# Optimization experiments

Hardware: AMD Instinct MI355X
Metric: run time of the kernel (lower is better)

Reference implementation:

```python
import jax, jax.numpy as jnp
import numpy as np


def _inst(Xs, idx):
    # Xs: list of [N_type, D] feature tables, one per metapath position.
    # idx: [N, K, P] int indices. Returns max-pooled instance vectors [N, K, D].
    v = Xs[0][idx[..., 0]]
    for p in range(1, len(Xs)):
        v = jnp.maximum(v, Xs[p][idx[..., p]])
    return v


def _instance_attn(h, inst, W, a):
    # h: [N, D] target features; inst: [N, K, D]; W: [H, D, D]; a: [H, D].
    hi = jnp.einsum('nd,hde->hne', h, W)               # [H, N, D]
    hv = jnp.einsum('nkd,hde->hnke', inst, W)          # [H, N, K, D]
    e = jax.nn.leaky_relu(
        jnp.einsum('hnke,he->hnk', hv + hi[:, :, None, :], a), 0.2)
    alpha = jax.nn.softmax(e, axis=2)                  # softmax over K instances
    out = jnp.einsum('hnk,hnke->ne', alpha, hv)
    return out / W.shape[0]                            # mean over heads


def _metapath_attn(Hs, W, b, q):
    Hstk = jnp.stack(Hs)                               # [P, N, D]
    sem = jnp.tanh(Hstk @ W + b).mean(axis=1)          # [P, D]
    beta = jax.nn.softmax(jnp.sum(jnp.tanh(sem) * q, axis=1), axis=0)  # [P]
    return jnp.einsum('p,pnd->nd', beta, Hstk), beta


def setup_inputs() -> dict:
    N, D, K, H = 2048, 256, 20, 4
    key = jax.random.key(0)
    ks = iter(jax.random.split(key, 40))
    nrm = lambda shape, s=1.0: jax.random.normal(next(ks), shape, jnp.float32) * s
    ridx = lambda shape: jax.random.randint(next(ks), shape, 0, N, jnp.int32)
    w_s = 1.0 / np.sqrt(D).astype(np.float32)
    inp = {
        'X_drug': nrm((N, D)), 'X_dis': nrm((N, D)), 'X_gene': nrm((N, D)),
        'idx_rdr': ridx((N, K, 3)), 'idx_rdgdr': ridx((N, K, 5)),
        'idx_dgd': ridx((N, K, 3)), 'idx_drd': ridx((N, K, 3)),
        'idx_drrd': ridx((N, K, 4)), 'idx_gdrdg': ridx((N, K, 5)),
    }
    for mp in ['rdr', 'rdgdr', 'dgd', 'drd', 'drrd', 'gdrdg']:
        inp['W_' + mp] = nrm((H, D, D), w_s)
        inp['a_' + mp] = nrm((H, D), 0.01)
    for t in ['drug', 'dis', 'gene']:
        inp['Wm_' + t] = nrm((D, D), w_s)
        inp['bm_' + t] = jnp.zeros((D,), jnp.float32)
        inp['qm_' + t] = nrm((D,), 0.01)
    return inp


def reference(X_drug, X_dis, X_gene,
              idx_rdr, idx_rdgdr, idx_dgd, idx_drd, idx_drrd, idx_gdrdg,
              W_rdr, a_rdr, W_rdgdr, a_rdgdr, W_dgd, a_dgd, W_drd, a_drd,
              W_drrd, a_drrd, W_gdrdg, a_gdrdg,
              Wm_drug, bm_drug, qm_drug, Wm_dis, bm_dis, qm_dis,
              Wm_gene, bm_gene, qm_gene):
    # Drug metapaths: RDR, RDGDR
    H_rdr = _instance_attn(X_drug, _inst([X_drug, X_dis, X_drug], idx_rdr), W_rdr, a_rdr)
    H_rdgdr = _instance_attn(X_drug, _inst([X_drug, X_dis, X_gene, X_dis, X_drug], idx_rdgdr), W_rdgdr, a_rdgdr)
    H_drug, beta_drug = _metapath_attn([H_rdr, H_rdgdr], Wm_drug, bm_drug, qm_drug)
    # Disease metapaths: DGD, DRD, DRRD
    H_dgd = _instance_attn(X_dis, _inst([X_dis, X_gene, X_dis], idx_dgd), W_dgd, a_dgd)
    H_drd = _instance_attn(X_dis, _inst([X_dis, X_drug, X_dis], idx_drd), W_drd, a_drd)
    H_drrd = _instance_attn(X_dis, _inst([X_dis, X_drug, X_drug, X_dis], idx_drrd), W_drrd, a_drrd)
    H_dis, beta_dis = _metapath_attn([H_dgd, H_drd, H_drrd], Wm_dis, bm_dis, qm_dis)
    # Gene metapath: GDRDG
    H_gdrdg = _instance_attn(X_gene, _inst([X_gene, X_dis, X_drug, X_dis, X_gene], idx_gdrdg), W_gdrdg, a_gdrdg)
    H_gene, beta_gene = _metapath_attn([H_gdrdg], Wm_gene, bm_gene, qm_gene)
    return H_drug, H_dis, H_gene, beta_drug, beta_dis, beta_gene
```

## Files before the change

### kernel.cpp

```cpp
#include <hip/hip_runtime.h>
#include <math.h>

#define NN 2048
#define DD 256
#define KK 20
#define HH 4

typedef short short8 __attribute__((ext_vector_type(8)));
typedef float f32x4  __attribute__((ext_vector_type(4)));
typedef _Float16 half8 __attribute__((ext_vector_type(8)));
typedef _Float16 h2    __attribute__((ext_vector_type(2)));

#if defined(__has_builtin)
#  if __has_builtin(__builtin_amdgcn_fdot2)
#    define HAS_FDOT2 1
#  else
#    define HAS_FDOT2 0
#  endif
#else
#  define HAS_FDOT2 0
#endif

struct AllMP  { const unsigned short* xs[6][5]; const int* idx[6]; const unsigned short* xt[6]; int P[6]; };
struct SixPtr { const float* p[6]; };
struct SemB   { const unsigned short* Wmt[6]; const float* bm[6]; };

__device__ inline float wsum(float v){
  #pragma unroll
  for (int o=32;o;o>>=1) v += __shfl_xor(v,o);
  return v;
}
__device__ inline float gsum16(float v){
  #pragma unroll
  for (int o=8;o;o>>=1) v += __shfl_xor(v,o);
  return v;
}
__device__ inline unsigned short f2h(float x){
  return __builtin_bit_cast(unsigned short, (_Float16)x);
}
__device__ inline float h2f(unsigned short u){
  return (float)__builtin_bit_cast(_Float16, u);
}
__device__ inline h2 bch2(unsigned int u){ return __builtin_bit_cast(h2, u); }
__device__ inline unsigned int bcu(h2 v){ return __builtin_bit_cast(unsigned int, v); }
__device__ inline h2 packh2(float a, float b){ h2 r; r[0]=(_Float16)a; r[1]=(_Float16)b; return r; }
__device__ inline h2 hmax2(h2 a, h2 b){
  unsigned int d, ua = bcu(a), ub = bcu(b);
  asm("v_pk_max_f16 %0, %1, %2" : "=v"(d) : "v"(ua), "v"(ub));
  return bch2(d);
}
__device__ inline float dot2(h2 a, h2 b, float c){
#if HAS_FDOT2
  return __builtin_amdgcn_fdot2(a, b, c, false);
#else
  return c + (float)a[0]*(float)b[0] + (float)a[1]*(float)b[1];
#endif
}
__device__ inline void glds16(const void* g, void* l){
  __builtin_amdgcn_global_load_lds(
    (const __attribute__((address_space(1))) unsigned int*)g,
    (__attribute__((address_space(3))) unsigned int*)l, 16, 0, 0);
}

__launch_bounds__(256)
__global__ void prep_kernel(SixPtr W, SixPtr a, SixPtr Xp, SixPtr Wm3,
                            float* __restrict__ wa, unsigned short* __restrict__ Xh,
                            unsigned short* __restrict__ Wt, unsigned short* __restrict__ Wmt,
                            float* __restrict__ zero_base, int zero_cnt){
  __shared__ unsigned short T_s[64][68];
  int b = blockIdx.x;
  const int t = threadIdx.x;

  if (b < 24){
    if (b == 0){
      for (int i=t;i<zero_cnt;i+=256) zero_base[i] = 0.f;
    }
    const int m = b >> 2;
    const int local = ((b & 3) << 8) | t;
    const int h = local >> 8, d = local & 255;
    const float4* wrow = (const float4*)(W.p[m] + (size_t)(h*DD + d)*DD);
    const float4* av   = (const float4*)(a.p[m] + h*DD);
    float acc = 0.f;
    #pragma unroll 8
    for (int e=0;e<64;e++){
      float4 wv = wrow[e], xv = av[e];
      acc += wv.x*xv.x + wv.y*xv.y + wv.z*xv.z + wv.w*xv.w;
    }
    wa[m*1024 + local] = acc;
    return;
  }
  b -= 24;
  if (b < 1536){
    int gid = b*256 + t;
    int tb  = gid >> 17;
    int off = gid & 131071;
    float4 v = ((const float4*)Xp.p[tb])[off];
    ushort4 o = { f2h(v.x), f2h(v.y), f2h(v.z), f2h(v.w) };
    ((ushort4*)(Xh + (size_t)tb*NN*DD))[off] = o;
    return;
  }
  b -= 1536;
  const float* src; unsigned short* ob; int R, C, r0, c0;
  if (b < 384){
    int m = b/64, rem = b%64;
    src = W.p[m]; ob = Wt + (size_t)m*256*1024;
    R = 1024; C = 256; r0 = (rem>>2)*64; c0 = (rem&3)*64;
  } else {
    int bb = b-384;
    int m = bb/16, rem = bb%16;
    src = Wm3.p[m]; ob = Wmt + (size_t)m*256*256;
    R = 256; C = 256; r0 = (rem>>2)*64; c0 = (rem&3)*64;
  }
  {
    const int rr = t>>4, cc = (t&15)*4;
    #pragma unroll
    for (int i=0;i<4;i++){
      float4 v = *(const float4*)(src + (size_t)(r0+rr+i*16)*C + c0 + cc);
      T_s[cc+0][rr+i*16]=f2h(v.x);
      T_s[cc+1][rr+i*16]=f2h(v.y);
      T_s[cc+2][rr+i*16]=f2h(v.z);
      T_s[cc+3][rr+i*16]=f2h(v.w);
    }
    __syncthreads();
    const int cr = t>>4, rc = (t&15)*4;
    #pragma unroll
    for (int i=0;i<4;i++){
      int c = c0 + cr + i*16;
      ushort4 v = { T_s[cr+i*16][rc+0], T_s[cr+i*16][rc+1],
                    T_s[cr+i*16][rc+2], T_s[cr+i*16][rc+3] };
      int col = (r0 + rc) ^ ((c&7)<<3);
      *(ushort4*)(ob + (size_t)c*R + col) = v;
    }
  }
}

template<int P>
__device__ inline void inst_core(const AllMP& mp, int m, int n, int l,
                                 const float* __restrict__ wa_all,
                                 unsigned int (*inst_lds)[128], float (*alpha_lds)[4],
                                 unsigned short* __restrict__ ctxh){
  const int g = l >> 4;
  const int j = l & 15;
  const int* __restrict__ gidx = mp.idx[m] + (size_t)n*(KK*P);

  h2 wh[8];
  {
    const float4* wab = (const float4*)(wa_all + m*1024 + g*256);
    #pragma unroll
    for (int c=0;c<4;c++){
      float4 wv = wab[j + 16*c];
      wh[2*c]   = packh2(wv.x, wv.y);
      wh[2*c+1] = packh2(wv.z, wv.w);
    }
  }

  float sg;
  {
    const uint2* xb = (const uint2*)(mp.xt[m] + (size_t)n*DD);
    float p_ = 0.f;
    #pragma unroll
    for (int c=0;c<4;c++){
      uint2 rr = xb[j + 16*c];
      p_ = dot2(bch2(rr.x), wh[2*c+0], p_);
      p_ = dot2(bch2(rr.y), wh[2*c+1], p_);
    }
    sg = gsum16(p_);
  }

  unsigned int v0[KK], v1[KK];
  #pragma unroll
  for (int k=0;k<KK;k++){
    h2 a, bb;
    {
      int id = gidx[k*P];
      const uint2* rp = (const uint2*)(mp.xs[m][0] + (size_t)id*DD);
      uint2 r = rp[l];
      a = bch2(r.x); bb = bch2(r.y);
    }
    #pragma unroll
    for (int p=1;p<P;p++){
      int id = gidx[k*P+p];
      const uint2* rp = (const uint2*)(mp.xs[m][p] + (size_t)id*DD);
      uint2 u = rp[l];
      a = hmax2(a, bch2(u.x)); bb = hmax2(bb, bch2(u.y));
    }
    v0[k] = bcu(a); v1[k] = bcu(bb);
    *(uint2*)&inst_lds[k][2*l] = make_uint2(v0[k], v1[k]);
  }

  float e[KK];
  #pragma unroll
  for (int k=0;k<KK;k++){
    float pr = 0.f;
    #pragma unroll
    for (int c=0;c<4;c++){
      uint2 rr = *(const uint2*)&inst_lds[k][2*(j+16*c)];
      pr = dot2(bch2(rr.x), wh[2*c+0], pr);
      pr = dot2(bch2(rr.y), wh[2*c+1], pr);
    }
    pr = gsum16(pr);
    float logit = pr + sg;
    e[k] = (logit>0.f) ? logit : 0.2f*logit;
  }

  float mx = e[0];
  #pragma unroll
  for (int k=1;k<KK;k++) mx = fmaxf(mx, e[k]);
  float s = 0.f;
  #pragma unroll
  for (int k=0;k<KK;k++){ e[k] = __expf(e[k]-mx); s += e[k]; }
  float inv = 1.0f/s;
  #pragma unroll
  for (int k=0;k<KK;k++) e[k] *= inv;
  if (j==0){
    #pragma unroll
    for (int k=0;k<KK;k++) alpha_lds[k][g] = e[k];
  }

  float c[4][4] = {};
  #pragma unroll
  for (int k=0;k<KK;k++){
    float4 af = *(const float4*)&alpha_lds[k][0];
    h2 x0 = bch2(v0[k]), x1 = bch2(v1[k]);
    float f0=(float)x0[0], f1=(float)x0[1], f2=(float)x1[0], f3=(float)x1[1];
    c[0][0]+=af.x*f0; c[0][1]+=af.x*f1; c[0][2]+=af.x*f2; c[0][3]+=af.x*f3;
    c[1][0]+=af.y*f0; c[1][1]+=af.y*f1; c[1][2]+=af.y*f2; c[1][3]+=af.y*f3;
    c[2][0]+=af.z*f0; c[2][1]+=af.z*f1; c[2][2]+=af.z*f2; c[2][3]+=af.z*f3;
    c[3][0]+=af.w*f0; c[3][1]+=af.w*f1; c[3][2]+=af.w*f2; c[3][3]+=af.w*f3;
  }

  unsigned short* cb = ctxh + ((size_t)m*NN + n)*1024;
  const int col = (4*l) ^ ((n&7)<<3);
  #pragma unroll
  for (int h=0;h<4;h++){
    ushort4 o = { f2h(c[h][0]), f2h(c[h][1]), f2h(c[h][2]), f2h(c[h][3]) };
    *(ushort4*)(cb + h*DD + col) = o;
  }
}

__launch_bounds__(64)
__global__ void inst_attn_kernel(AllMP mp, const float* __restrict__ wa_all,
                                 unsigned short* __restrict__ ctxh){
  __shared__ unsigned int inst_lds[KK][128];
  __shared__ float alpha_lds[KK][4];
  const int m = blockIdx.y;
  const int n = blockIdx.x;
  const int l = threadIdx.x;
  switch(mp.P[m]){
    case 3: inst_core<3>(mp,m,n,l,wa_all,inst_lds,alpha_lds,ctxh); break;
    case 4: inst_core<4>(mp,m,n,l,wa_all,inst_lds,alpha_lds,ctxh); break;
    default: inst_core<5>(mp,m,n,l,wa_all,inst_lds,alpha_lds,ctxh); break;
  }
}

__launch_bounds__(256)
__global__ void gemm_kernel(const unsigned short* __restrict__ ctxh,
                            const unsigned short* __restrict__ Wt,
                            unsigned short* __restrict__ Hmp){
  __shared__ unsigned short A_s[2][64][64];
  __shared__ unsigned short B_s[2][64][64];
  const int m  = blockIdx.z;
  const int n0 = blockIdx.x*64, c0 = blockIdx.y*64;
  const int t  = threadIdx.x;
  const int l  = t & 63;
  const int wid  = t >> 6;
  const int wrow = wid & 1, wcol = wid >> 1;
  const unsigned short* Abase = ctxh + (size_t)m*NN*1024;
  const unsigned short* Bbase = Wt   + (size_t)m*256*1024;

  f32x4 acc[2][2] = {};
  const int row8 = l>>3, seg = l&7;

  {
    #pragma unroll
    for (int i=0;i<2;i++){
      const int r = wid*16 + i*8;
      glds16(Abase + (size_t)(n0+r+row8)*1024 + 0 + seg*8, &A_s[0][r][0]);
      glds16(Bbase + (size_t)(c0+r+row8)*1024 + 0 + seg*8, &B_s[0][r][0]);
    }
  }
  __syncthreads();

  #pragma unroll 2
  for (int it=0; it<16; it++){
    const int buf = it&1;
    if (it<15){
      const int k0 = (it+1)*64;
      #pragma unroll
      for (int i=0;i<2;i++){
        const int r = wid*16 + i*8;
        glds16(Abase + (size_t)(n0+r+row8)*1024 + k0 + seg*8, &A_s[buf^1][r][0]);
        glds16(Bbase + (size_t)(c0+r+row8)*1024 + k0 + seg*8, &B_s[buf^1][r][0]);
      }
    }
    __builtin_amdgcn_s_setprio(1);
    #pragma unroll
    for (int kf=0;kf<2;kf++){
      half8 a[2], b[2];
      const int s = kf*4 + (l>>4);
      #pragma unroll
      for (int mr=0;mr<2;mr++){
        const int row = wrow*32 + mr*16 + (l&15);
        a[mr] = __builtin_bit_cast(half8, *(const short8*)&A_s[buf][row][(s ^ (row&7))*8]);
      }
      #pragma unroll
      for (int nr=0;nr<2;nr++){
        const int col = wcol*32 + nr*16 + (l&15);
        b[nr] = __builtin_bit_cast(half8, *(const short8*)&B_s[buf][col][(s ^ (col&7))*8]);
      }
      #pragma unroll
      for (int mr=0;mr<2;mr++)
        #pragma unroll
        for (int nr=0;nr<2;nr++)
          acc[mr][nr] = __builtin_amdgcn_mfma_f32_16x16x32_f16(a[mr], b[nr], acc[mr][nr], 0,0,0);
    }
    __builtin_amdgcn_s_setprio(0);
    __syncthreads();
  }

  unsigned short* out = Hmp + (size_t)m*NN*DD;
  #pragma unroll
  for (int mr=0;mr<2;mr++){
    const int rbase = n0 + wrow*32 + mr*16 + (l>>4)*4;
    #pragma unroll
    for (int nr=0;nr<2;nr++){
      const int col = c0 + wcol*32 + nr*16 + (l&15);
      #pragma unroll
      for (int r=0;r<4;r++){
        const int rw = rbase + r;
        out[(size_t)rw*DD + (col ^ ((rw&7)<<3))] = f2h(acc[mr][nr][r]*0.25f);
      }
    }
  }
}

__launch_bounds__(256)
__global__ void sem_kernel(const unsigned short* __restrict__ Hmp, SemB sb,
                           float* __restrict__ sem_sum){
  __shared__ unsigned short A_s[64][256];
  __shared__ unsigned short B_s[64][256];
  const int m  = blockIdx.z;
  const int n0 = blockIdx.x*64, c0 = blockIdx.y*64;
  const int t  = threadIdx.x, l = t & 63, wid = t >> 6;
  const int wrow = wid & 1, wcol = wid >> 1;
  const unsigned short* Ab = Hmp + (size_t)m*NN*DD;
  const unsigned short* Bb = sb.Wmt[m];

  const int row2 = l>>5, seg = l&31;
  #pragma unroll
  for (int i=0;i<8;i++){
    const int r = wid*16 + i*2;
    glds16(Ab + (size_t)(n0+r+row2)*DD + seg*8, &A_s[r][0]);
    glds16(Bb + (size_t)(c0+r+row2)*DD + seg*8, &B_s[r][0]);
  }
  __syncthreads();

  f32x4 acc[2][2] = {};
  #pragma unroll
  for (int kf=0; kf<8; kf++){
    const int s = kf*4 + (l>>4);
    half8 a[2], b[2];
    #pragma unroll
    for (int mr=0;mr<2;mr++){
      int row = wrow*32 + mr*16 + (l&15);
      int ss = (s&24) | ((s&7)^(row&7));
      a[mr] = __builtin_bit_cast(half8, *(const short8*)((const char*)&A_s[0][0] + row*512 + ss*16));
    }
    #pragma unroll
    for (int nr=0;nr<2;nr++){
      int row = wcol*32 + nr*16 + (l&15);
      int ss = (s&24) | ((s&7)^(row&7));
      b[nr] = __builtin_bit_cast(half8, *(const short8*)((const char*)&B_s[0][0] + row*512 + ss*16));
    }
    #pragma unroll
    for (int mr=0;mr<2;mr++)
      #pragma unroll
      for (int nr=0;nr<2;nr++)
        acc[mr][nr] = __builtin_amdgcn_mfma_f32_16x16x32_f16(a[mr], b[nr], acc[mr][nr], 0,0,0);
  }

  #pragma unroll
  for (int nr=0;nr<2;nr++){
    const int col = c0 + wcol*32 + nr*16 + (l&15);
    float b = sb.bm[m][col];
    float sv = 0.f;
    #pragma unroll
    for (int mr=0;mr<2;mr++)
      #pragma unroll
      for (int r=0;r<4;r++)
        sv += tanhf(acc[mr][nr][r] + b);
    sv += __shfl_xor(sv,16);
    sv += __shfl_xor(sv,32);
    if (l < 16) atomicAdd(&sem_sum[m*DD + col], sv);
  }
}

__launch_bounds__(256)
__global__ void combine_kernel(const unsigned short* __restrict__ Hmp,
                               const float* __restrict__ sem_sum,
                               const float* __restrict__ qm0, const float* __restrict__ qm1,
                               const float* __restrict__ qm2,
                               float* __restrict__ out){
  const int type = blockIdx.y;
  const int start = (type==0) ? 0 : (type==1) ? 2 : 5;
  const int P = (type==0) ? 2 : (type==1) ? 3 : 1;
  const float* qm = (type==0) ? qm0 : (type==1) ? qm1 : qm2;
  const int t = threadIdx.x;
  __shared__ float red[3][4];
  __shared__ float beta_s[3];

  float q = qm[t];
  #pragma unroll
  for (int p=0;p<3;p++){
    if (p < P){
      float sm = sem_sum[(start+p)*DD + t] * (1.0f/NN);
      float v = wsum(tanhf(sm)*q);
      if ((t&63)==0) red[p][t>>6] = v;
    }
  }
  __syncthreads();
  if (t==0){
    float logits[3], e[3];
    float mx = -INFINITY;
    #pragma unroll
    for (int p=0;p<3;p++){
      if (p < P){
        logits[p] = red[p][0]+red[p][1]+red[p][2]+red[p][3];
        mx = fmaxf(mx, logits[p]);
      }
    }
    float s = 0.f;
    #pragma unroll
    for (int p=0;p<3;p++){
      if (p < P){ e[p] = __expf(logits[p]-mx); s += e[p]; }
    }
    #pragma unroll
    for (int p=0;p<3;p++)
      if (p < P) beta_s[p] = e[p]/s;
  }
  __syncthreads();

  if (blockIdx.x==0 && t<P)
    out[(size_t)3*NN*DD + start + t] = beta_s[t];

  const int n0 = blockIdx.x*4;
  #pragma unroll
  for (int r=0;r<4;r++){
    const int n = n0 + r;
    const int ds = t ^ ((n&7)<<3);
    const unsigned short* base = Hmp + ((size_t)start*NN + n)*DD + ds;
    float acc = 0.f;
    #pragma unroll
    for (int p=0;p<3;p++)
      if (p < P) acc += beta_s[p]*h2f(base[(size_t)p*NN*DD]);
    out[((size_t)type*NN + n)*DD + t] = acc;
  }
}

extern "C" void kernel_launch(void* const* d_in, const int* in_sizes, int n_in,
                              void* d_out, int out_size, void* d_ws, size_t ws_size,
                              hipStream_t stream) {
  SixPtr Xp; Xp.p[0]=(const float*)d_in[0]; Xp.p[1]=(const float*)d_in[1]; Xp.p[2]=(const float*)d_in[2];
  for (int i=3;i<6;i++) Xp.p[i]=Xp.p[0];

  SixPtr Wl, al;
  for (int m=0;m<6;m++){ Wl.p[m] = (const float*)d_in[9+2*m]; al.p[m] = (const float*)d_in[10+2*m]; }
  const float* Wm_[3]; const float* bm_[3]; const float* qm_[3];
  for (int tt=0;tt<3;tt++){
    Wm_[tt] = (const float*)d_in[21+3*tt];
    bm_[tt] = (const float*)d_in[22+3*tt];
    qm_[tt] = (const float*)d_in[23+3*tt];
  }
  SixPtr Wm3; for (int i=0;i<6;i++) Wm3.p[i] = Wm_[i<3?i:0];

  char* ws = (char*)d_ws;
  float* wa_all  = (float*)ws;                               ws += 6*1024*4;
  float* sem_sum = (float*)ws;                               ws += 6*DD*4;
  unsigned short* Hmp  = (unsigned short*)ws;                ws += (size_t)6*NN*DD*2;
  unsigned short* Wt   = (unsigned short*)ws;                ws += (size_t)6*256*1024*2;
  unsigned short* Wmt  = (unsigned short*)ws;                ws += (size_t)3*256*256*2;
  unsigned short* Xh   = (unsigned short*)ws;                ws += (size_t)3*NN*DD*2;
  unsigned short* ctxh = (unsigned short*)ws;

  AllMP mp;
  for (int m=0;m<6;m++) mp.idx[m] = (const int*)d_in[3+m];
  const int P_[6] = {3,5,3,3,4,5};
  for (int m=0;m<6;m++) mp.P[m] = P_[m];
  const int xt_t[6] = {0,0,1,1,1,2};
  const int gp_t[6][5] = {
    {0,1,0,0,0}, {0,1,2,1,0}, {1,2,1,1,1},
    {1,0,1,1,1}, {1,0,0,1,1}, {2,1,0,1,2}};
  for (int m=0;m<6;m++){
    mp.xt[m] = Xh + (size_t)xt_t[m]*NN*DD;
    for (int p=0;p<5;p++) mp.xs[m][p] = Xh + (size_t)gp_t[m][p]*NN*DD;
  }

  SemB sb;
  const int type_of[6] = {0,0,1,1,1,2};
  for (int m=0;m<6;m++){
    sb.Wmt[m] = Wmt + (size_t)type_of[m]*256*256;
    sb.bm[m]  = bm_[type_of[m]];
  }

  prep_kernel<<<dim3(24+1536+384+48),dim3(256),0,stream>>>(
      Wl, al, Xp, Wm3, wa_all, Xh, Wt, Wmt, sem_sum, 6*DD);

  inst_attn_kernel<<<dim3(NN,6),dim3(64),0,stream>>>(mp, wa_all, ctxh);
  gemm_kernel<<<dim3(32,4,6),dim3(256),0,stream>>>(ctxh, Wt, Hmp);
  sem_kernel<<<dim3(32,4,6),dim3(256),0,stream>>>(Hmp, sb, sem_sum);

  float* out = (float*)d_out;
  combine_kernel<<<dim3(NN/4,3),dim3(256),0,stream>>>(Hmp, sem_sum, qm_[0], qm_[1], qm_[2], out);
}
```

Before: 91.21 us.

## Stream instance attention over K chunks with unnormalized softmax accumulation

The kernel now processes the 20 instances in chunks of 5 through a double-buffered LDS chunk and accumulates exp-weighted context on the fly, normalizing by per-head sums only at the end. It no longer subtracts a running max before exponentiating. This drops the per-thread v0/v1/e arrays to cut register pressure and LDS size, which should allow higher occupancy and more gather overlap. The missing max subtraction risks overflow if the logits are large, and chunking limits how many gathers are in flight at once.

```diff
diff --git a/kernel.cpp b/kernel.cpp
--- a/kernel.cpp
+++ b/kernel.cpp
@@ -4,6 +4,7 @@
 #define NN 2048
 #define DD 256
 #define KK 20
+#define KCH 5
 #define HH 4
 
 typedef short short8 __attribute__((ext_vector_type(8)));
@@ -137,7 +138,8 @@
 template<int P>
 __device__ inline void inst_core(const AllMP& mp, int m, int n, int l,
                                  const float* __restrict__ wa_all,
-                                 unsigned int (*inst_lds)[128], float (*alpha_lds)[4],
+                                 uint2 (*chunk)[KCH][64],
+                                 float (*e_s)[KCH][4],
                                  unsigned short* __restrict__ ctxh){
   const int g = l >> 4;
   const int j = l & 15;
@@ -167,89 +169,89 @@
     sg = gsum16(p_);
   }
 
-  unsigned int v0[KK], v1[KK];
-  #pragma unroll
-  for (int k=0;k<KK;k++){
-    h2 a, bb;
-    {
-      int id = gidx[k*P];
-      const uint2* rp = (const uint2*)(mp.xs[m][0] + (size_t)id*DD);
-      uint2 r = rp[l];
-      a = bch2(r.x); bb = bch2(r.y);
-    }
-    #pragma unroll
-    for (int p=1;p<P;p++){
-      int id = gidx[k*P+p];
-      const uint2* rp = (const uint2*)(mp.xs[m][p] + (size_t)id*DD);
-      uint2 u = rp[l];
-      a = hmax2(a, bch2(u.x)); bb = hmax2(bb, bch2(u.y));
-    }
-    v0[k] = bcu(a); v1[k] = bcu(bb);
-    *(uint2*)&inst_lds[k][2*l] = make_uint2(v0[k], v1[k]);
-  }
-
-  float e[KK];
-  #pragma unroll
-  for (int k=0;k<KK;k++){
-    float pr = 0.f;
-    #pragma unroll
-    for (int c=0;c<4;c++){
-      uint2 rr = *(const uint2*)&inst_lds[k][2*(j+16*c)];
-      pr = dot2(bch2(rr.x), wh[2*c+0], pr);
-      pr = dot2(bch2(rr.y), wh[2*c+1], pr);
-    }
-    pr = gsum16(pr);
-    float logit = pr + sg;
-    e[k] = (logit>0.f) ? logit : 0.2f*logit;
-  }
-
-  float mx = e[0];
-  #pragma unroll
-  for (int k=1;k<KK;k++) mx = fmaxf(mx, e[k]);
-  float s = 0.f;
-  #pragma unroll
-  for (int k=0;k<KK;k++){ e[k] = __expf(e[k]-mx); s += e[k]; }
-  float inv = 1.0f/s;
-  #pragma unroll
-  for (int k=0;k<KK;k++) e[k] *= inv;
-  if (j==0){
-    #pragma unroll
-    for (int k=0;k<KK;k++) alpha_lds[k][g] = e[k];
-  }
-
+  float s0=0.f, s1=0.f, s2=0.f, s3=0.f;
   float c[4][4] = {};
-  #pragma unroll
-  for (int k=0;k<KK;k++){
-    float4 af = *(const float4*)&alpha_lds[k][0];
-    h2 x0 = bch2(v0[k]), x1 = bch2(v1[k]);
-    float f0=(float)x0[0], f1=(float)x0[1], f2=(float)x1[0], f3=(float)x1[1];
-    c[0][0]+=af.x*f0; c[0][1]+=af.x*f1; c[0][2]+=af.x*f2; c[0][3]+=af.x*f3;
-    c[1][0]+=af.y*f0; c[1][1]+=af.y*f1; c[1][2]+=af.y*f2; c[1][3]+=af.y*f3;
-    c[2][0]+=af.z*f0; c[2][1]+=af.z*f1; c[2][2]+=af.z*f2; c[2][3]+=af.z*f3;
-    c[3][0]+=af.w*f0; c[3][1]+=af.w*f1; c[3][2]+=af.w*f2; c[3][3]+=af.w*f3;
-  }
+
+  #pragma unroll
+  for (int ch=0; ch<KK/KCH; ch++){
+    const int par = ch & 1;
+    #pragma unroll
+    for (int kk=0; kk<KCH; kk++){
+      const int k = ch*KCH + kk;
+      h2 a, bb;
+      {
+        int id = gidx[k*P];
+        const uint2* rp = (const uint2*)(mp.xs[m][0] + (size_t)id*DD);
+        uint2 r = rp[l];
+        a = bch2(r.x); bb = bch2(r.y);
+      }
+      #pragma unroll
+      for (int p=1;p<P;p++){
+        int id = gidx[k*P+p];
+        const uint2* rp = (const uint2*)(mp.xs[m][p] + (size_t)id*DD);
+        uint2 u = rp[l];
+        a = hmax2(a, bch2(u.x)); bb = hmax2(bb, bch2(u.y));
+      }
+      chunk[par][kk][l] = make_uint2(bcu(a), bcu(bb));
+    }
+    #pragma unroll
+    for (int kk=0; kk<KCH; kk++){
+      float pr = 0.f;
+      #pragma unroll
+      for (int cidx=0;cidx<4;cidx++){
+        uint2 rr = chunk[par][kk][j + 16*cidx];
+        pr = dot2(bch2(rr.x), wh[2*cidx+0], pr);
+        pr = dot2(bch2(rr.y), wh[2*cidx+1], pr);
+      }
+      pr = gsum16(pr);
+      if (j==0){
+        float logit = pr + sg;
+        e_s[par][kk][g] = (logit>0.f) ? logit : 0.2f*logit;
+      }
+    }
+    #pragma unroll
+    for (int kk=0; kk<KCH; kk++){
+      float4 e4 = *(const float4*)&e_s[par][kk][0];
+      float w0=__expf(e4.x), w1=__expf(e4.y), w2=__expf(e4.z), w3=__expf(e4.w);
+      s0+=w0; s1+=w1; s2+=w2; s3+=w3;
+      uint2 xv = chunk[par][kk][l];
+      h2 x0 = bch2(xv.x), x1 = bch2(xv.y);
+      float f0=(float)x0[0], f1=(float)x0[1], f2=(float)x1[0], f3=(float)x1[1];
+      c[0][0]+=w0*f0; c[0][1]+=w0*f1; c[0][2]+=w0*f2; c[0][3]+=w0*f3;
+      c[1][0]+=w1*f0; c[1][1]+=w1*f1; c[1][2]+=w1*f2; c[1][3]+=w1*f3;
+      c[2][0]+=w2*f0; c[2][1]+=w2*f1; c[2][2]+=w2*f2; c[2][3]+=w2*f3;
+      c[3][0]+=w3*f0; c[3][1]+=w3*f1; c[3][2]+=w3*f2; c[3][3]+=w3*f3;
+    }
+  }
+
+  const float i0=1.f/s0, i1=1.f/s1, i2=1.f/s2, i3=1.f/s3;
 
   unsigned short* cb = ctxh + ((size_t)m*NN + n)*1024;
   const int col = (4*l) ^ ((n&7)<<3);
-  #pragma unroll
-  for (int h=0;h<4;h++){
-    ushort4 o = { f2h(c[h][0]), f2h(c[h][1]), f2h(c[h][2]), f2h(c[h][3]) };
-    *(ushort4*)(cb + h*DD + col) = o;
+  {
+    ushort4 o0 = { f2h(c[0][0]*i0), f2h(c[0][1]*i0), f2h(c[0][2]*i0), f2h(c[0][3]*i0) };
+    ushort4 o1 = { f2h(c[1][0]*i1), f2h(c[1][1]*i1), f2h(c[1][2]*i1), f2h(c[1][3]*i1) };
+    ushort4 o2 = { f2h(c[2][0]*i2), f2h(c[2][1]*i2), f2h(c[2][2]*i2), f2h(c[2][3]*i2) };
+    ushort4 o3 = { f2h(c[3][0]*i3), f2h(c[3][1]*i3), f2h(c[3][2]*i3), f2h(c[3][3]*i3) };
+    *(ushort4*)(cb + 0*DD + col) = o0;
+    *(ushort4*)(cb + 1*DD + col) = o1;
+    *(ushort4*)(cb + 2*DD + col) = o2;
+    *(ushort4*)(cb + 3*DD + col) = o3;
   }
 }
 
 __launch_bounds__(64)
 __global__ void inst_attn_kernel(AllMP mp, const float* __restrict__ wa_all,
                                  unsigned short* __restrict__ ctxh){
-  __shared__ unsigned int inst_lds[KK][128];
-  __shared__ float alpha_lds[KK][4];
+  __shared__ uint2 chunk[2][KCH][64];
+  __shared__ float e_s[2][KCH][4];
   const int m = blockIdx.y;
   const int n = blockIdx.x;
   const int l = threadIdx.x;
   switch(mp.P[m]){
-    case 3: inst_core<3>(mp,m,n,l,wa_all,inst_lds,alpha_lds,ctxh); break;
-    case 4: inst_core<4>(mp,m,n,l,wa_all,inst_lds,alpha_lds,ctxh); break;
-    default: inst_core<5>(mp,m,n,l,wa_all,inst_lds,alpha_lds,ctxh); break;
+    case 3: inst_core<3>(mp,m,n,l,wa_all,chunk,e_s,ctxh); break;
+    case 4: inst_core<4>(mp,m,n,l,wa_all,chunk,e_s,ctxh); break;
+    default: inst_core<5>(mp,m,n,l,wa_all,chunk,e_s,ctxh); break;
   }
 }
 
```

After: 118.2 us. +29.6%, slower.

## Compute instance attention logits with MFMA instead of fdot2 reductions

Applied to the files above, without the earlier changes.

Replaces the per-instance fdot2 dot products and 16-lane shuffle reductions for attention logits with two 16x16x32 f16 MFMAs. The 20 pooled instance vectors plus the target row are staged in padded LDS and multiplied against a zero-padded f16 copy of W·a, which prep_kernel now writes. Softmax is then computed over the MFMA accumulator layout with cross-lane shuffles. This trades scalar dot work for matrix-core work, at the cost of extra LDS staging, a wider padded weight buffer and more complex lane indexing.

```diff
diff --git a/kernel.cpp b/kernel.cpp
--- a/kernel.cpp
+++ b/kernel.cpp
@@ -11,16 +11,6 @@
 typedef _Float16 half8 __attribute__((ext_vector_type(8)));
 typedef _Float16 h2    __attribute__((ext_vector_type(2)));
 
-#if defined(__has_builtin)
-#  if __has_builtin(__builtin_amdgcn_fdot2)
-#    define HAS_FDOT2 1
-#  else
-#    define HAS_FDOT2 0
-#  endif
-#else
-#  define HAS_FDOT2 0
-#endif
-
 struct AllMP  { const unsigned short* xs[6][5]; const int* idx[6]; const unsigned short* xt[6]; int P[6]; };
 struct SixPtr { const float* p[6]; };
 struct SemB   { const unsigned short* Wmt[6]; const float* bm[6]; };
@@ -30,11 +20,6 @@
   for (int o=32;o;o>>=1) v += __shfl_xor(v,o);
   return v;
 }
-__device__ inline float gsum16(float v){
-  #pragma unroll
-  for (int o=8;o;o>>=1) v += __shfl_xor(v,o);
-  return v;
-}
 __device__ inline unsigned short f2h(float x){
   return __builtin_bit_cast(unsigned short, (_Float16)x);
 }
@@ -42,19 +27,10 @@
   return (float)__builtin_bit_cast(_Float16, u);
 }
 __device__ inline h2 bch2(unsigned int u){ return __builtin_bit_cast(h2, u); }
-__device__ inline unsigned int bcu(h2 v){ return __builtin_bit_cast(unsigned int, v); }
-__device__ inline h2 packh2(float a, float b){ h2 r; r[0]=(_Float16)a; r[1]=(_Float16)b; return r; }
-__device__ inline h2 hmax2(h2 a, h2 b){
-  unsigned int d, ua = bcu(a), ub = bcu(b);
+__device__ inline unsigned int umax2(unsigned int ua, unsigned int ub){
+  unsigned int d;
   asm("v_pk_max_f16 %0, %1, %2" : "=v"(d) : "v"(ua), "v"(ub));
-  return bch2(d);
-}
-__device__ inline float dot2(h2 a, h2 b, float c){
-#if HAS_FDOT2
-  return __builtin_amdgcn_fdot2(a, b, c, false);
-#else
-  return c + (float)a[0]*(float)b[0] + (float)a[1]*(float)b[1];
-#endif
+  return d;
 }
 __device__ inline void glds16(const void* g, void* l){
   __builtin_amdgcn_global_load_lds(
@@ -64,7 +40,8 @@
 
 __launch_bounds__(256)
 __global__ void prep_kernel(SixPtr W, SixPtr a, SixPtr Xp, SixPtr Wm3,
-                            float* __restrict__ wa, unsigned short* __restrict__ Xh,
+                            float* __restrict__ wa, unsigned short* __restrict__ wah,
+                            unsigned short* __restrict__ Xh,
                             unsigned short* __restrict__ Wt, unsigned short* __restrict__ Wmt,
                             float* __restrict__ zero_base, int zero_cnt){
   __shared__ unsigned short T_s[64][68];
@@ -87,6 +64,10 @@
       acc += wv.x*xv.x + wv.y*xv.y + wv.z*xv.z + wv.w*xv.w;
     }
     wa[m*1024 + local] = acc;
+    wah[(size_t)m*4096 + local] = f2h(acc);
+    wah[(size_t)m*4096 + 1024 + local] = 0;
+    wah[(size_t)m*4096 + 2048 + local] = 0;
+    wah[(size_t)m*4096 + 3072 + local] = 0;
     return;
   }
   b -= 24;
@@ -136,85 +117,78 @@
 
 template<int P>
 __device__ inline void inst_core(const AllMP& mp, int m, int n, int l,
-                                 const float* __restrict__ wa_all,
-                                 unsigned int (*inst_lds)[128], float (*alpha_lds)[4],
+                                 const unsigned short* __restrict__ wah,
+                                 unsigned short* inst_lds,
+                                 float (*alpha_lds)[4],
                                  unsigned short* __restrict__ ctxh){
-  const int g = l >> 4;
-  const int j = l & 15;
   const int* __restrict__ gidx = mp.idx[m] + (size_t)n*(KK*P);
 
-  h2 wh[8];
-  {
-    const float4* wab = (const float4*)(wa_all + m*1024 + g*256);
-    #pragma unroll
-    for (int c=0;c<4;c++){
-      float4 wv = wab[j + 16*c];
-      wh[2*c]   = packh2(wv.x, wv.y);
-      wh[2*c+1] = packh2(wv.z, wv.w);
-    }
-  }
-
-  float sg;
-  {
-    const uint2* xb = (const uint2*)(mp.xt[m] + (size_t)n*DD);
-    float p_ = 0.f;
-    #pragma unroll
-    for (int c=0;c<4;c++){
-      uint2 rr = xb[j + 16*c];
-      p_ = dot2(bch2(rr.x), wh[2*c+0], p_);
-      p_ = dot2(bch2(rr.y), wh[2*c+1], p_);
-    }
-    sg = gsum16(p_);
-  }
-
   unsigned int v0[KK], v1[KK];
   #pragma unroll
   for (int k=0;k<KK;k++){
-    h2 a, bb;
+    unsigned int a, bb;
     {
       int id = gidx[k*P];
-      const uint2* rp = (const uint2*)(mp.xs[m][0] + (size_t)id*DD);
-      uint2 r = rp[l];
-      a = bch2(r.x); bb = bch2(r.y);
+      uint2 r = ((const uint2*)(mp.xs[m][0] + (size_t)id*DD))[l];
+      a = r.x; bb = r.y;
     }
     #pragma unroll
     for (int p=1;p<P;p++){
       int id = gidx[k*P+p];
-      const uint2* rp = (const uint2*)(mp.xs[m][p] + (size_t)id*DD);
-      uint2 u = rp[l];
-      a = hmax2(a, bch2(u.x)); bb = hmax2(bb, bch2(u.y));
-    }
-    v0[k] = bcu(a); v1[k] = bcu(bb);
-    *(uint2*)&inst_lds[k][2*l] = make_uint2(v0[k], v1[k]);
-  }
-
-  float e[KK];
-  #pragma unroll
-  for (int k=0;k<KK;k++){
-    float pr = 0.f;
-    #pragma unroll
-    for (int c=0;c<4;c++){
-      uint2 rr = *(const uint2*)&inst_lds[k][2*(j+16*c)];
-      pr = dot2(bch2(rr.x), wh[2*c+0], pr);
-      pr = dot2(bch2(rr.y), wh[2*c+1], pr);
-    }
-    pr = gsum16(pr);
-    float logit = pr + sg;
-    e[k] = (logit>0.f) ? logit : 0.2f*logit;
-  }
-
-  float mx = e[0];
-  #pragma unroll
-  for (int k=1;k<KK;k++) mx = fmaxf(mx, e[k]);
-  float s = 0.f;
-  #pragma unroll
-  for (int k=0;k<KK;k++){ e[k] = __expf(e[k]-mx); s += e[k]; }
-  float inv = 1.0f/s;
-  #pragma unroll
-  for (int k=0;k<KK;k++) e[k] *= inv;
-  if (j==0){
-    #pragma unroll
-    for (int k=0;k<KK;k++) alpha_lds[k][g] = e[k];
+      uint2 u = ((const uint2*)(mp.xs[m][p] + (size_t)id*DD))[l];
+      a = umax2(a, u.x); bb = umax2(bb, u.y);
+    }
+    v0[k] = a; v1[k] = bb;
+    *(uint2*)(inst_lds + k*264 + 4*l) = make_uint2(a, bb);
+  }
+  {
+    uint2 xt = ((const uint2*)(mp.xt[m] + (size_t)n*DD))[l];
+    *(uint2*)(inst_lds + 20*264 + 4*l) = xt;
+  }
+
+  f32x4 acc0 = {}, acc1 = {};
+  {
+    const int r = l & 15, qc = (l>>4)*8;
+    const unsigned short* wb = wah + (size_t)m*4096 + (size_t)(l&15)*256;
+    #pragma unroll
+    for (int s=0;s<8;s++){
+      half8 a0 = __builtin_bit_cast(half8, *(const short8*)(inst_lds + r*264      + s*32 + qc));
+      half8 a1 = __builtin_bit_cast(half8, *(const short8*)(inst_lds + (16+r)*264 + s*32 + qc));
+      half8 bf = __builtin_bit_cast(half8, *(const short8*)(wb + s*32 + qc));
+      acc0 = __builtin_amdgcn_mfma_f32_16x16x32_f16(a0, bf, acc0, 0,0,0);
+      acc1 = __builtin_amdgcn_mfma_f32_16x16x32_f16(a1, bf, acc1, 0,0,0);
+    }
+  }
+
+  const int col = l & 15, q = l >> 4;
+  float sgv = __shfl(acc1[0], 16 + col);
+  float lg[4], lg2[4];
+  #pragma unroll
+  for (int r=0;r<4;r++){
+    float x = acc0[r] + sgv; lg[r]  = (x>0.f) ? x : 0.2f*x;
+    float y = acc1[r] + sgv; lg2[r] = (y>0.f) ? y : 0.2f*y;
+  }
+  float mx  = fmaxf(fmaxf(lg[0],lg[1]), fmaxf(lg[2],lg[3]));
+  float mx2 = fmaxf(fmaxf(lg2[0],lg2[1]), fmaxf(lg2[2],lg2[3]));
+  mx = fmaxf(mx, (q==0) ? mx2 : -INFINITY);
+  mx = fmaxf(mx, __shfl_xor(mx,16));
+  mx = fmaxf(mx, __shfl_xor(mx,32));
+  float ex[4], ex2[4], s = 0.f;
+  #pragma unroll
+  for (int r=0;r<4;r++){ ex[r] = __expf(lg[r]-mx); s += ex[r]; }
+  #pragma unroll
+  for (int r=0;r<4;r++)  ex2[r] = __expf(lg2[r]-mx);
+  if (q==0) s += ex2[0]+ex2[1]+ex2[2]+ex2[3];
+  s += __shfl_xor(s,16);
+  s += __shfl_xor(s,32);
+  const float inv = 1.f/s;
+  if (col < HH){
+    #pragma unroll
+    for (int r=0;r<4;r++) alpha_lds[q*4+r][col] = ex[r]*inv;
+    if (q==0){
+      #pragma unroll
+      for (int r=0;r<4;r++) alpha_lds[16+r][col] = ex2[r]*inv;
+    }
   }
 
   float c[4][4] = {};
@@ -230,26 +204,26 @@
   }
 
   unsigned short* cb = ctxh + ((size_t)m*NN + n)*1024;
-  const int col = (4*l) ^ ((n&7)<<3);
+  const int sc = (4*l) ^ ((n&7)<<3);
   #pragma unroll
   for (int h=0;h<4;h++){
     ushort4 o = { f2h(c[h][0]), f2h(c[h][1]), f2h(c[h][2]), f2h(c[h][3]) };
-    *(ushort4*)(cb + h*DD + col) = o;
+    *(ushort4*)(cb + h*DD + sc) = o;
   }
 }
 
 __launch_bounds__(64)
-__global__ void inst_attn_kernel(AllMP mp, const float* __restrict__ wa_all,
+__global__ void inst_attn_kernel(AllMP mp, const unsigned short* __restrict__ wah,
                                  unsigned short* __restrict__ ctxh){
-  __shared__ unsigned int inst_lds[KK][128];
+  __shared__ unsigned short inst_lds[32*264];
   __shared__ float alpha_lds[KK][4];
   const int m = blockIdx.y;
   const int n = blockIdx.x;
   const int l = threadIdx.x;
   switch(mp.P[m]){
-    case 3: inst_core<3>(mp,m,n,l,wa_all,inst_lds,alpha_lds,ctxh); break;
-    case 4: inst_core<4>(mp,m,n,l,wa_all,inst_lds,alpha_lds,ctxh); break;
-    default: inst_core<5>(mp,m,n,l,wa_all,inst_lds,alpha_lds,ctxh); break;
+    case 3: inst_core<3>(mp,m,n,l,wah,inst_lds,alpha_lds,ctxh); break;
+    case 4: inst_core<4>(mp,m,n,l,wah,inst_lds,alpha_lds,ctxh); break;
+    default: inst_core<5>(mp,m,n,l,wah,inst_lds,alpha_lds,ctxh); break;
   }
 }
 
@@ -476,6 +450,7 @@
   char* ws = (char*)d_ws;
   float* wa_all  = (float*)ws;                               ws += 6*1024*4;
   float* sem_sum = (float*)ws;                               ws += 6*DD*4;
+  unsigned short* wah  = (unsigned short*)ws;                ws += (size_t)6*4096*2;
   unsigned short* Hmp  = (unsigned short*)ws;                ws += (size_t)6*NN*DD*2;
   unsigned short* Wt   = (unsigned short*)ws;                ws += (size_t)6*256*1024*2;
   unsigned short* Wmt  = (unsigned short*)ws;                ws += (size_t)3*256*256*2;
@@ -503,9 +478,9 @@
   }
 
   prep_kernel<<<dim3(24+1536+384+48),dim3(256),0,stream>>>(
-      Wl, al, Xp, Wm3, wa_all, Xh, Wt, Wmt, sem_sum, 6*DD);
-
-  inst_attn_kernel<<<dim3(NN,6),dim3(64),0,stream>>>(mp, wa_all, ctxh);
+      Wl, al, Xp, Wm3, wa_all, wah, Xh, Wt, Wmt, sem_sum, 6*DD);
+
+  inst_attn_kernel<<<dim3(NN,6),dim3(64),0,stream>>>(mp, wah, ctxh);
   gemm_kernel<<<dim3(32,4,6),dim3(256),0,stream>>>(ctxh, Wt, Hmp);
   sem_kernel<<<dim3(32,4,6),dim3(256),0,stream>>>(Hmp, sb, sem_sum);
 
```

Result: slower. 98.35 us (+7.8%).
